# Kernel optimization log

Hardware: AMD Instinct MI355X
Metric: run time of the kernel (lower is better)

## Reference

```python
import jax, jax.numpy as jnp
import numpy as np
import math

N, M_KV = 8192, 8192
QDIM, KDIM, MID = 256, 256, 128
NEG_BIG = -float(1 << 32)  # matches torch.masked_fill(Attn, mask, -(1 << 32))


def setup_inputs() -> dict:
    key = jax.random.key(0)
    ks = jax.random.split(key, 8)
    main_feat = jax.random.normal(ks[0], (N, QDIM), dtype=jnp.float32)
    other_feat = jax.random.normal(ks[1], (M_KV, KDIM), dtype=jnp.float32)
    fix_feat = jax.random.uniform(ks[2], (M_KV,), dtype=jnp.float32)
    mask = jax.random.randint(ks[3], (N, M_KV), 0, 2).astype(jnp.bool_)
    # Linear params (torch.nn.Linear stores weight as [out, in])
    Wq = jax.random.normal(ks[4], (MID, QDIM), dtype=jnp.float32) / math.sqrt(QDIM)
    bq = jax.random.normal(ks[5], (MID,), dtype=jnp.float32) * 0.01
    Wk = jax.random.normal(ks[6], (MID, KDIM), dtype=jnp.float32) / math.sqrt(KDIM)
    bk = jax.random.normal(ks[7], (MID,), dtype=jnp.float32) * 0.01
    return {"main_feat": main_feat, "other_feat": other_feat, "fix_feat": fix_feat,
            "mask": mask, "Wq": Wq, "bq": bq, "Wk": Wk, "bk": bk}


def reference(main_feat, other_feat, fix_feat, mask, Wq, bq, Wk, bk):
    # Projections: y = x @ W.T + b
    Q = main_feat @ Wq.T + bq            # [N, MID]
    K = other_feat @ Wk.T + bk           # [M, MID]
    scale = 1.0 / math.sqrt(MID)
    attn = jnp.einsum('nd,md->nm', Q, K) * scale   # [N, M]
    attn = jnp.where(mask, NEG_BIG, attn)
    attn = jax.nn.softmax(attn, axis=-1)
    # diag(fix_feat) @ other_feat is just a row-wise scale of V
    V = fix_feat[:, None] * other_feat   # [M, KDIM]
    return attn @ V                      # [N, KDIM]
```

## Files before the change

### kernel.cpp

```cpp
#include <hip/hip_runtime.h>
#include <hip/hip_bf16.h>
#include <stdint.h>

typedef __attribute__((ext_vector_type(8))) short short8;
typedef __attribute__((ext_vector_type(4))) float floatx4;

#define MFMA32K(a, b, c) __builtin_amdgcn_mfma_f32_16x16x32_bf16(a, b, c, 0, 0, 0)

constexpr int N_Q  = 8192;
constexpr int M_KV = 8192;
constexpr int DMID = 128;
constexpr int DV   = 256;

__device__ __forceinline__ unsigned short f2bf(float x) {
    unsigned u = __float_as_uint(x);
    u += 0x7fffu + ((u >> 16) & 1u);
    return (unsigned short)(u >> 16);
}

__device__ __forceinline__ short8 cvt_f8_bf8(float4 a, float4 b) {
    short8 r;
    r[0] = (short)f2bf(a.x); r[1] = (short)f2bf(a.y);
    r[2] = (short)f2bf(a.z); r[3] = (short)f2bf(a.w);
    r[4] = (short)f2bf(b.x); r[5] = (short)f2bf(b.y);
    r[6] = (short)f2bf(b.z); r[7] = (short)f2bf(b.w);
    return r;
}

__device__ __forceinline__ void gl_lds16(const unsigned short* g, unsigned short* l) {
    __builtin_amdgcn_global_load_lds(
        (const __attribute__((address_space(1))) unsigned int*)g,
        (__attribute__((address_space(3))) unsigned int*)l, 16, 0, 0);
}

__device__ __forceinline__ unsigned nz4(unsigned x) {
    unsigned nz = (((x & 0x7f7f7f7fu) + 0x7f7f7f7fu) | x) & 0x80808080u;
    unsigned a = (nz >> 7) & 0x01010101u;
    return (a * 0x01020408u) >> 24;
}

__global__ __launch_bounds__(256) void proj_kernel(
    const float* __restrict__ main_feat, const float* __restrict__ Wq, const float* __restrict__ bq,
    const float* __restrict__ other_feat, const float* __restrict__ Wk, const float* __restrict__ bk,
    unsigned short* __restrict__ Qw, unsigned short* __restrict__ Kw)
{
    const float* src;  const float* W;  const float* bias;  unsigned short* dst;
    if (blockIdx.y == 0) { src = main_feat;  W = Wq; bias = bq; dst = Qw; }
    else                 { src = other_feat; W = Wk; bias = bk; dst = Kw; }

    const int wave = threadIdx.x >> 6, lane = threadIdx.x & 63;
    const int n = lane & 15, quad = lane >> 4;
    const int row0 = blockIdx.x * 64 + wave * 16;

    short8 a[8];
    const float* ap = src + (size_t)(row0 + n) * 256 + quad * 8;
#pragma unroll
    for (int ks = 0; ks < 8; ++ks) {
        float4 x0 = *(const float4*)(ap + ks * 32);
        float4 x1 = *(const float4*)(ap + ks * 32 + 4);
        a[ks] = cvt_f8_bf8(x0, x1);
    }

    floatx4 acc[8];
#pragma unroll
    for (int nt = 0; nt < 8; ++nt) acc[nt] = floatx4{0.f, 0.f, 0.f, 0.f};

#pragma unroll
    for (int nt = 0; nt < 8; ++nt) {
        const float* wp = W + (size_t)(nt * 16 + n) * 256 + quad * 8;
#pragma unroll
        for (int ks = 0; ks < 8; ++ks) {
            float4 w0 = *(const float4*)(wp + ks * 32);
            float4 w1 = *(const float4*)(wp + ks * 32 + 4);
            short8 b = cvt_f8_bf8(w0, w1);
            acc[nt] = MFMA32K(a[ks], b, acc[nt]);
        }
    }

#pragma unroll
    for (int nt = 0; nt < 8; ++nt) {
        float bb = bias[nt * 16 + n];
#pragma unroll
        for (int reg = 0; reg < 4; ++reg) {
            int r = row0 + quad * 4 + reg;
            int c = nt * 16 + n;
            int phys = ((((c >> 3) + r) & 15) << 3) | (c & 7);
            dst[(size_t)r * DMID + phys] = f2bf(acc[nt][reg] + bb);
        }
    }
}

__global__ __launch_bounds__(256) void build_vt_kernel(
    const float* __restrict__ other_feat, const float* __restrict__ fix_feat,
    unsigned short* __restrict__ Vt)
{
    __shared__ unsigned short tile[64 * 72];
    const int t = threadIdx.x;
    const int m0 = blockIdx.x * 64, d0 = blockIdx.y * 64;

#pragma unroll
    for (int r = 0; r < 4; ++r) {
        int idx = r * 256 + t;
        int ml = idx >> 4, dl4 = (idx & 15) * 4;
        float4 v = *(const float4*)(other_feat + (size_t)(m0 + ml) * 256 + d0 + dl4);
        float f = fix_feat[m0 + ml];
        tile[(dl4 + 0) * 72 + ml] = f2bf(v.x * f);
        tile[(dl4 + 1) * 72 + ml] = f2bf(v.y * f);
        tile[(dl4 + 2) * 72 + ml] = f2bf(v.z * f);
        tile[(dl4 + 3) * 72 + ml] = f2bf(v.w * f);
    }
    __syncthreads();
#pragma unroll
    for (int r = 0; r < 8; ++r) {
        int dl = r * 8 + (t >> 5);
        int d = d0 + dl;
        int ml = (t & 31) * 2;
        int e = ml >> 5, s = (ml >> 4) & 1, q = (ml >> 2) & 3, j = ml & 3;
        int pc = e * 32 + q * 8 + s * 4 + j;
        int phys = ((((pc >> 3) + d) & 7) << 3) | (pc & 7);
        unsigned int v0 = tile[dl * 72 + ml];
        unsigned int v1 = tile[dl * 72 + ml + 1];
        *(unsigned int*)(Vt + (size_t)d * M_KV + m0 + phys) = v0 | (v1 << 16);
    }
}

template<int ESZ>
__device__ __forceinline__ void flash_body(
    const unsigned short* __restrict__ Qw, const unsigned short* __restrict__ Kw,
    const unsigned short* __restrict__ Vt, const unsigned int* __restrict__ mask,
    unsigned short* __restrict__ Opart, float* __restrict__ Lpart,
    int nsplit, int lgNs,
    unsigned short* k_lds , unsigned short* vt_lds )
{
    const int L = blockIdx.x + gridDim.x * blockIdx.y;
    const int ly = L & (nsplit - 1);
    const int lx = L >> lgNs;
    const int chunkLen = M_KV >> lgNs;
    const int mBeg = ly * chunkLen;
    const int iters = chunkLen / 64;
    const int phase = lx & (iters - 1);
    const int tid = threadIdx.x;
    const int wave = tid >> 6, lane = tid & 63, n = lane & 15, quad = lane >> 4;
    const int qrow0 = lx * 128 + wave * 16;
    constexpr float SC = 0.08838834764831845f * 1.4426950408889634f;

    auto mcol = [&](int it) {
        int idx = it + phase;
        if (idx >= iters) idx -= iters;
        return mBeg + idx * 64;
    };

    short8 qf[4];
#pragma unroll
    for (int db = 0; db < 4; ++db) {
        int row = qrow0 + n;
        int phys = (db * 4 + quad + row) & 15;
        qf[db] = *(const short8*)(Qw + (size_t)row * DMID + phys * 8);
    }

    floatx4 Oacc[16];
#pragma unroll
    for (int dt = 0; dt < 16; ++dt) Oacc[dt] = floatx4{0.f, 0.f, 0.f, 0.f};

    float lrow = 0.f;

    const unsigned short* kg = Kw + (size_t)(wave * 4 + (lane >> 4)) * DMID + (lane & 15) * 8;
    const unsigned short* vg = Vt + (size_t)(wave * 8 + (lane >> 3)) * M_KV + (lane & 7) * 8;
    const int kqn = quad + n;

    uint4    mv4[4];
    unsigned mv1[4];

    auto load_mask = [&](int m0l) {
        const size_t row = (size_t)(qrow0 + n);
        if constexpr (ESZ == 4) {
            const unsigned* mp = mask + row * M_KV + m0l + quad * 4;
#pragma unroll
            for (int kvt = 0; kvt < 4; ++kvt)
                mv4[kvt] = *(const uint4*)(mp + kvt * 16);
        } else {
            const unsigned* mp = mask + row * (M_KV / 4) + (m0l >> 2) + quad;
#pragma unroll
            for (int kvt = 0; kvt < 4; ++kvt)
                mv1[kvt] = mp[kvt * 4];
        }
    };

#pragma unroll
    for (int r = 0; r < 2; ++r)
        gl_lds16(kg + (size_t)(mcol(0) + r * 32) * DMID, &k_lds[wave * 512 + r * 4096]);
    __builtin_amdgcn_sched_barrier(0);
    load_mask(mcol(0));
    __builtin_amdgcn_sched_barrier(0);
    asm volatile("s_waitcnt vmcnt(4)\n\ts_barrier" ::: "memory");

    for (int it = 0; it < iters; ++it) {
        const int m0 = mcol(it);
        const unsigned short* kbuf = k_lds + (it & 1) * 8192;

#pragma unroll
        for (int r = 0; r < 4; ++r)
            gl_lds16(vg + (size_t)(r * 64) * M_KV + m0, &vt_lds[wave * 512 + r * 4096]);
        const bool more = (it + 1 < iters);
        if (more) {
            const int m1 = mcol(it + 1);
            unsigned short* knext = k_lds + ((it + 1) & 1) * 8192 + wave * 512;
#pragma unroll
            for (int r = 0; r < 2; ++r)
                gl_lds16(kg + (size_t)(m1 + r * 32) * DMID, knext + r * 4096);
        }
        __builtin_amdgcn_sched_barrier(0);

        unsigned wq = 0;
        if constexpr (ESZ == 4) {
#pragma unroll
            for (int kvt = 0; kvt < 4; ++kvt) {
                const unsigned* c = (const unsigned*)&mv4[kvt];
#pragma unroll
                for (int j = 0; j < 4; ++j)
                    wq |= (c[j] != 0u ? 1u : 0u) << (kvt * 4 + j);
            }
        } else {
#pragma unroll
            for (int kvt = 0; kvt < 4; ++kvt)
                wq |= nz4(mv1[kvt]) << (kvt * 4);
        }
        __builtin_amdgcn_sched_barrier(0);

        if (more) load_mask(mcol(it + 1));
        __builtin_amdgcn_sched_barrier(0);

        floatx4 ST[4];
        __builtin_amdgcn_s_setprio(1);
#pragma unroll
        for (int kvt = 0; kvt < 4; ++kvt) {
            const int rowoff = (kvt * 16 + n) * DMID;
            short8 a0 = *(const short8*)&kbuf[rowoff + (((kqn + 0) & 15) << 3)];
            short8 a1 = *(const short8*)&kbuf[rowoff + (((kqn + 4) & 15) << 3)];
            short8 a2 = *(const short8*)&kbuf[rowoff + (((kqn + 8) & 15) << 3)];
            short8 a3 = *(const short8*)&kbuf[rowoff + (((kqn + 12) & 15) << 3)];
            floatx4 s = floatx4{0.f, 0.f, 0.f, 0.f};
            s = MFMA32K(a0, qf[0], s);
            s = MFMA32K(a1, qf[1], s);
            s = MFMA32K(a2, qf[2], s);
            s = MFMA32K(a3, qf[3], s);
            ST[kvt] = s;
        }
        __builtin_amdgcn_s_setprio(0);

        short8 pf8[2];
#pragma unroll
        for (int kvt = 0; kvt < 4; ++kvt) {
            int e = kvt >> 1, s = kvt & 1;
            float p[4];
#pragma unroll
            for (int j = 0; j < 4; ++j) {
                float v = __builtin_amdgcn_exp2f(ST[kvt][j] * SC);
                p[j] = ((wq >> (kvt * 4 + j)) & 1u) ? 0.f : v;
                lrow += p[j];
            }
            __hip_bfloat162 h0 = __float22bfloat162_rn(make_float2(p[0], p[1]));
            __hip_bfloat162 h1 = __float22bfloat162_rn(make_float2(p[2], p[3]));
            unsigned u0, u1;
            __builtin_memcpy(&u0, &h0, 4);
            __builtin_memcpy(&u1, &h1, 4);
            ((unsigned*)&pf8[e])[s * 2 + 0] = u0;
            ((unsigned*)&pf8[e])[s * 2 + 1] = u1;
        }

        if (more)
            asm volatile("s_waitcnt vmcnt(4) lgkmcnt(0)\n\ts_barrier" ::: "memory");
        else
            asm volatile("s_waitcnt vmcnt(0) lgkmcnt(0)\n\ts_barrier" ::: "memory");

        __builtin_amdgcn_s_setprio(1);
#pragma unroll
        for (int e = 0; e < 2; ++e) {
#pragma unroll
            for (int dt = 0; dt < 16; ++dt) {
                const int vb = (dt * 16 + n) * 64 + (((e * 4 + quad + n) & 7) << 3);
                short8 bv = *(const short8*)&vt_lds[vb];
                Oacc[dt] = MFMA32K(pf8[e], bv, Oacc[dt]);
            }
        }
        __builtin_amdgcn_s_setprio(0);

        asm volatile("s_waitcnt lgkmcnt(0)\n\ts_barrier" ::: "memory");
    }

    const size_t obase = (size_t)ly * N_Q * DV;
#pragma unroll
    for (int dt = 0; dt < 16; ++dt)
#pragma unroll
        for (int reg = 0; reg < 4; ++reg) {
            int gr = qrow0 + quad * 4 + reg;
            Opart[obase + (size_t)gr * DV + dt * 16 + n] = f2bf(Oacc[dt][reg]);
        }
    {
        float r = lrow;
        r += __shfl_xor(r, 16);
        r += __shfl_xor(r, 32);
        if (quad == 0)
            Lpart[ly * N_Q + qrow0 + n] = r;
    }
}

__global__ __launch_bounds__(512, 2) void flash_kernel(
    const unsigned short* __restrict__ Qw, const unsigned short* __restrict__ Kw,
    const unsigned short* __restrict__ Vt, const unsigned int* __restrict__ mask,
    unsigned short* __restrict__ Opart, float* __restrict__ Lpart,
    int nsplit, int lgNs)
{
    __shared__ __align__(16) unsigned short k_lds[2][64 * 128];
    __shared__ __align__(16) unsigned short vt_lds[256 * 64];

    unsigned w0 = mask[threadIdx.x & 63];
    bool isf = (w0 == 0x3f800000u);
    bool isb = (w0 > 1u) && !isf;
    bool wide = (__ballot(isf) != 0ull) || (__ballot(isb) == 0ull);

    if (wide)
        flash_body<4>(Qw, Kw, Vt, mask, Opart, Lpart, nsplit, lgNs,
                      &k_lds[0][0], vt_lds);
    else
        flash_body<1>(Qw, Kw, Vt, mask, Opart, Lpart, nsplit, lgNs,
                      &k_lds[0][0], vt_lds);
}

__global__ __launch_bounds__(256) void combine_kernel(
    const unsigned short* __restrict__ Opart, const float* __restrict__ Lpart,
    float* __restrict__ out, int nsplit)
{
    const int row = blockIdx.x, d = threadIdx.x;
    float L = 0.f, o = 0.f;
    for (int c = 0; c < nsplit; ++c) {
        L += Lpart[c * N_Q + row];
        unsigned int b = Opart[((size_t)c * N_Q + row) * DV + d];
        o += __uint_as_float(b << 16);
    }
    out[(size_t)row * DV + d] = o / L;
}

extern "C" void kernel_launch(void* const* d_in, const int* in_sizes, int n_in,
                              void* d_out, int out_size, void* d_ws, size_t ws_size,
                              hipStream_t stream)
{
    const float* main_feat  = (const float*)d_in[0];
    const float* other_feat = (const float*)d_in[1];
    const float* fix_feat   = (const float*)d_in[2];
    const void*  mask       = d_in[3];
    const float* Wq         = (const float*)d_in[4];
    const float* bq         = (const float*)d_in[5];
    const float* Wk         = (const float*)d_in[6];
    const float* bk         = (const float*)d_in[7];
    float* out = (float*)d_out;

    char* ws = (char*)d_ws;
    unsigned short* Qw = (unsigned short*)(ws);
    unsigned short* Kw = (unsigned short*)(ws + (1ull << 21));
    unsigned short* Vt = (unsigned short*)(ws + (2ull << 21));
    float* Lpart = (float*)(ws + (16ull << 20) + 2048);

    const size_t base = (16ull << 20) + 2048;
    auto need = [&](int ns) {
        return base + (size_t)ns * N_Q * 4 + (size_t)ns * N_Q * DV * 2;
    };
    int nsplit = 1, lgNs = 0;
    if (ws_size >= need(8))      { nsplit = 8; lgNs = 3; }
    else if (ws_size >= need(4)) { nsplit = 4; lgNs = 2; }
    else if (ws_size >= need(2)) { nsplit = 2; lgNs = 1; }

    unsigned short* Opart = (unsigned short*)(Lpart + (size_t)nsplit * N_Q);

    hipLaunchKernelGGL(proj_kernel, dim3(128, 2), dim3(256), 0, stream,
                       main_feat, Wq, bq, other_feat, Wk, bk, Qw, Kw);
    hipLaunchKernelGGL(build_vt_kernel, dim3(128, 4), dim3(256), 0, stream,
                       other_feat, fix_feat, Vt);
    hipLaunchKernelGGL(flash_kernel, dim3(64, nsplit), dim3(512), 0, stream,
                       Qw, Kw, Vt, (const unsigned int*)mask, Opart, Lpart, nsplit, lgNs);
    hipLaunchKernelGGL(combine_kernel, dim3(N_Q), dim3(256), 0, stream,
                       Opart, Lpart, out, nsplit);
}
```

Before: 423.2 us.

## Triple-buffer V tiles in LDS, prefetch one step ahead, drop trailing barrier

V-transpose tiles are now spread over three LDS buffers and issued one iteration ahead, together with the next K tile, instead of at the start of the current iteration. This hides V global-load latency behind the QK and softmax work of the current step. Rotating through three buffers makes it safe to remove the end-of-iteration barrier. The cost is LDS per block growing from 64KB to 128KB, which likely allows only one 512-thread block per CU instead of two and cuts latency hiding across blocks.

```diff
diff --git a/kernel.cpp b/kernel.cpp
--- a/kernel.cpp
+++ b/kernel.cpp
@@ -185,29 +185,35 @@
                 mv1[kvt] = mp[kvt * 4];
         }
     };
-
-#pragma unroll
-    for (int r = 0; r < 2; ++r)
-        gl_lds16(kg + (size_t)(mcol(0) + r * 32) * DMID, &k_lds[wave * 512 + r * 4096]);
+    auto issue_vt = [&](int m0l, int buf) {
+#pragma unroll
+        for (int r = 0; r < 4; ++r)
+            gl_lds16(vg + (size_t)(r * 64) * M_KV + m0l,
+                     &vt_lds[buf * 16384 + wave * 512 + r * 4096]);
+    };
+    auto issue_k = [&](int m0l, int buf) {
+#pragma unroll
+        for (int r = 0; r < 2; ++r)
+            gl_lds16(kg + (size_t)(m0l + r * 32) * DMID,
+                     &k_lds[buf * 8192 + wave * 512 + r * 4096]);
+    };
+
+    issue_vt(mcol(0), 0);
+    issue_k(mcol(0), 0);
     __builtin_amdgcn_sched_barrier(0);
     load_mask(mcol(0));
     __builtin_amdgcn_sched_barrier(0);
     asm volatile("s_waitcnt vmcnt(4)\n\ts_barrier" ::: "memory");
 
+    int vcur = 0;
     for (int it = 0; it < iters; ++it) {
-        const int m0 = mcol(it);
         const unsigned short* kbuf = k_lds + (it & 1) * 8192;
-
-#pragma unroll
-        for (int r = 0; r < 4; ++r)
-            gl_lds16(vg + (size_t)(r * 64) * M_KV + m0, &vt_lds[wave * 512 + r * 4096]);
+        const int vnext = (vcur == 2) ? 0 : vcur + 1;
         const bool more = (it + 1 < iters);
+
         if (more) {
-            const int m1 = mcol(it + 1);
-            unsigned short* knext = k_lds + ((it + 1) & 1) * 8192 + wave * 512;
-#pragma unroll
-            for (int r = 0; r < 2; ++r)
-                gl_lds16(kg + (size_t)(m1 + r * 32) * DMID, knext + r * 4096);
+            issue_vt(mcol(it + 1), vnext);
+            issue_k(mcol(it + 1), (it + 1) & 1);
         }
         __builtin_amdgcn_sched_barrier(0);
 
@@ -273,19 +279,20 @@
         else
             asm volatile("s_waitcnt vmcnt(0) lgkmcnt(0)\n\ts_barrier" ::: "memory");
 
+        const unsigned short* vbuf = vt_lds + vcur * 16384;
         __builtin_amdgcn_s_setprio(1);
 #pragma unroll
         for (int e = 0; e < 2; ++e) {
 #pragma unroll
             for (int dt = 0; dt < 16; ++dt) {
                 const int vb = (dt * 16 + n) * 64 + (((e * 4 + quad + n) & 7) << 3);
-                short8 bv = *(const short8*)&vt_lds[vb];
+                short8 bv = *(const short8*)&vbuf[vb];
                 Oacc[dt] = MFMA32K(pf8[e], bv, Oacc[dt]);
             }
         }
         __builtin_amdgcn_s_setprio(0);
 
-        asm volatile("s_waitcnt lgkmcnt(0)\n\ts_barrier" ::: "memory");
+        vcur = vnext;
     }
 
     const size_t obase = (size_t)ly * N_Q * DV;
@@ -312,7 +319,7 @@
     int nsplit, int lgNs)
 {
     __shared__ __align__(16) unsigned short k_lds[2][64 * 128];
-    __shared__ __align__(16) unsigned short vt_lds[256 * 64];
+    __shared__ __align__(16) unsigned short vt_lds[3][256 * 64];
 
     unsigned w0 = mask[threadIdx.x & 63];
     bool isf = (w0 == 0x3f800000u);
@@ -321,10 +328,10 @@
 
     if (wide)
         flash_body<4>(Qw, Kw, Vt, mask, Opart, Lpart, nsplit, lgNs,
-                      &k_lds[0][0], vt_lds);
+                      &k_lds[0][0], &vt_lds[0][0]);
     else
         flash_body<1>(Qw, Kw, Vt, mask, Opart, Lpart, nsplit, lgNs,
-                      &k_lds[0][0], vt_lds);
+                      &k_lds[0][0], &vt_lds[0][0]);
 }
 
 __global__ __launch_bounds__(256) void combine_kernel(
```

Result: slower. 433.3 us (+2.4%).
